# Kernel tuning notes

Measured on AMD Instinct MI355X. Metric: run time of the kernel, lower is better.

The kernel has to match this reference:

```python
import jax, jax.numpy as jnp
import numpy as np

NUM_HASHES = 4
EMBEDDING_DIM = 256
K = 512
B_TABLE = 256  # self.B


def setup_inputs() -> dict:
    key = jax.random.key(0)
    k1, k2, k3 = jax.random.split(key, 3)
    x = jax.random.randint(k1, (16, 4096, NUM_HASHES), 0, K, dtype=jnp.int64)
    # nn.Embedding(K*num_hashes + num_hashes, 1)
    weight_table = jax.random.normal(k2, (K * NUM_HASHES + NUM_HASHES, 1), dtype=jnp.float32)
    # nn.EmbeddingBag(B+1, embedding_dim)
    emb_table = jax.random.normal(k3, (B_TABLE + 1, EMBEDDING_DIM), dtype=jnp.float32)
    return {"x": x, "weight_table": weight_table, "emb_table": emb_table}


def reference(x, weight_table, emb_table):
    # x: [batch, seq, num_hashes] int in [0, K)
    num_hashes = x.shape[-1]
    indices = x // 2                                   # [b, s, h] in [0, 256]
    offsets = jnp.arange(num_hashes, dtype=x.dtype) * (K + 1)
    weight_idx = x + offsets                           # [b, s, h]
    w = weight_table[weight_idx, 0]                    # [b, s, h] per-sample weights
    e = emb_table[indices]                             # [b, s, h, d]
    # EmbeddingBag mode='sum' with per_sample_weights: weighted sum over hashes
    return jnp.einsum('bsh,bshd->bsd', w, e)
```

## Files before the change

kernel.cpp:

```cpp
#include <hip/hip_runtime.h>

#define NUM_HASHES 4
#define DIM 256

typedef float v4f __attribute__((ext_vector_type(4)));

__global__ __launch_bounds__(256) void HashEmbedding_44976897523736_kernel(
    const int* __restrict__ x,
    const float* __restrict__ wt,
    const float* __restrict__ emb,
    float* __restrict__ out,
    int num_pos, int num_waves)
{
    const int lane = threadIdx.x & 63;
    const int wave = __builtin_amdgcn_readfirstlane(
        blockIdx.x * (blockDim.x >> 6) + (threadIdx.x >> 6));

    #pragma unroll 2
    for (int p = wave; p < num_pos; p += num_waves) {
        const int4 xi = *reinterpret_cast<const int4*>(x + p * NUM_HASHES);
        const int i0 = __builtin_amdgcn_readfirstlane(xi.x);
        const int i1 = __builtin_amdgcn_readfirstlane(xi.y);
        const int i2 = __builtin_amdgcn_readfirstlane(xi.z);
        const int i3 = __builtin_amdgcn_readfirstlane(xi.w);

        const float w0 = wt[i0];
        const float w1 = wt[i1 + 513];
        const float w2 = wt[i2 + 1026];
        const float w3 = wt[i3 + 1539];

        const v4f e0 = reinterpret_cast<const v4f*>(emb + (i0 >> 1) * DIM)[lane];
        const v4f e1 = reinterpret_cast<const v4f*>(emb + (i1 >> 1) * DIM)[lane];
        const v4f e2 = reinterpret_cast<const v4f*>(emb + (i2 >> 1) * DIM)[lane];
        const v4f e3 = reinterpret_cast<const v4f*>(emb + (i3 >> 1) * DIM)[lane];

        v4f r = w0 * e0 + w1 * e1 + w2 * e2 + w3 * e3;

        __builtin_nontemporal_store(
            r, reinterpret_cast<v4f*>(out + (size_t)p * DIM) + lane);
    }
}

extern "C" void kernel_launch(void* const* d_in, const int* in_sizes, int n_in,
                              void* d_out, int out_size, void* d_ws, size_t ws_size,
                              hipStream_t stream) {
    const int*   x   = (const int*)d_in[0];
    const float* wt  = (const float*)d_in[1];
    const float* emb = (const float*)d_in[2];
    float*       out = (float*)d_out;

    const int num_pos = in_sizes[0] / NUM_HASHES;

    const int block = 256;
    int blocks = 2048;
    int num_waves = blocks * (block / 64);
    if (num_waves > num_pos) {
        blocks = (num_pos * 64 + block - 1) / block;
        if (blocks < 1) blocks = 1;
        num_waves = blocks * (block / 64);
    }

    HashEmbedding_44976897523736_kernel<<<blocks, block, 0, stream>>>(
        x, wt, emb, out, num_pos, num_waves);
}
```

Baseline: 85.18 us.

## Stage embedding table slices in LDS and split output columns across blocks

Each block loads a 64-column slice of the embedding table into shared memory and serves gathers from LDS, with blocks split across four column slices. This aims to replace global/L2 gather traffic with LDS reads. In exchange, index and weight loads are repeated per slice, stores narrow to scalar floats, and the large LDS footprint with 1024-thread blocks limits occupancy.

```diff
diff --git a/kernel.cpp b/kernel.cpp
--- a/kernel.cpp
+++ b/kernel.cpp
@@ -2,22 +2,39 @@
 
 #define NUM_HASHES 4
 #define DIM 256
+#define SLICE 64
+#define NSLICES (DIM / SLICE)
+#define LDS_ROWS 256
+#define BLOCK 1024
+#define WPB (BLOCK / 64)
 
-typedef float v4f __attribute__((ext_vector_type(4)));
-
-__global__ __launch_bounds__(256) void HashEmbedding_44976897523736_kernel(
+__global__ __launch_bounds__(BLOCK) void HashEmbedding_44976897523736_kernel(
     const int* __restrict__ x,
     const float* __restrict__ wt,
     const float* __restrict__ emb,
     float* __restrict__ out,
-    int num_pos, int num_waves)
+    int num_pos, int waves_per_slice)
 {
-    const int lane = threadIdx.x & 63;
-    const int wave = __builtin_amdgcn_readfirstlane(
-        blockIdx.x * (blockDim.x >> 6) + (threadIdx.x >> 6));
+    __shared__ float tbl[LDS_ROWS * SLICE];
 
-    #pragma unroll 2
-    for (int p = wave; p < num_pos; p += num_waves) {
+    const int tid   = threadIdx.x;
+    const int lane  = tid & 63;
+    const int slice = blockIdx.x & (NSLICES - 1);
+    const int chunk = blockIdx.x >> 2;
+
+    const float* esrc = emb + slice * SLICE;
+    #pragma unroll
+    for (int i = tid; i < LDS_ROWS * SLICE; i += BLOCK) {
+        const int r = i >> 6;
+        const int c = i & (SLICE - 1);
+        tbl[i] = esrc[r * DIM + c];
+    }
+    __syncthreads();
+
+    const int wave = __builtin_amdgcn_readfirstlane(chunk * WPB + (tid >> 6));
+
+    #pragma unroll 4
+    for (int p = wave; p < num_pos; p += waves_per_slice) {
         const int4 xi = *reinterpret_cast<const int4*>(x + p * NUM_HASHES);
         const int i0 = __builtin_amdgcn_readfirstlane(xi.x);
         const int i1 = __builtin_amdgcn_readfirstlane(xi.y);
@@ -29,15 +46,15 @@
         const float w2 = wt[i2 + 1026];
         const float w3 = wt[i3 + 1539];
 
-        const v4f e0 = reinterpret_cast<const v4f*>(emb + (i0 >> 1) * DIM)[lane];
-        const v4f e1 = reinterpret_cast<const v4f*>(emb + (i1 >> 1) * DIM)[lane];
-        const v4f e2 = reinterpret_cast<const v4f*>(emb + (i2 >> 1) * DIM)[lane];
-        const v4f e3 = reinterpret_cast<const v4f*>(emb + (i3 >> 1) * DIM)[lane];
+        const float e0 = tbl[(i0 >> 1) * SLICE + lane];
+        const float e1 = tbl[(i1 >> 1) * SLICE + lane];
+        const float e2 = tbl[(i2 >> 1) * SLICE + lane];
+        const float e3 = tbl[(i3 >> 1) * SLICE + lane];
 
-        v4f r = w0 * e0 + w1 * e1 + w2 * e2 + w3 * e3;
+        const float r = w0 * e0 + w1 * e1 + w2 * e2 + w3 * e3;
 
         __builtin_nontemporal_store(
-            r, reinterpret_cast<v4f*>(out + (size_t)p * DIM) + lane);
+            r, out + (size_t)p * DIM + slice * SLICE + lane);
     }
 }
 
@@ -51,15 +68,14 @@
 
     const int num_pos = in_sizes[0] / NUM_HASHES;
 
-    const int block = 256;
-    int blocks = 2048;
-    int num_waves = blocks * (block / 64);
-    if (num_waves > num_pos) {
-        blocks = (num_pos * 64 + block - 1) / block;
-        if (blocks < 1) blocks = 1;
-        num_waves = blocks * (block / 64);
+    int chunks = 128;
+    if (chunks * WPB > num_pos) {
+        chunks = (num_pos + WPB - 1) / WPB;
+        if (chunks < 1) chunks = 1;
     }
+    const int waves_per_slice = chunks * WPB;
+    const int blocks = chunks * NSLICES;
 
-    HashEmbedding_44976897523736_kernel<<<blocks, block, 0, stream>>>(
-        x, wt, emb, out, num_pos, num_waves);
+    HashEmbedding_44976897523736_kernel<<<blocks, BLOCK, 0, stream>>>(
+        x, wt, emb, out, num_pos, waves_per_slice);
 }
```

Result: slower. 99.74 us (+17.1%).

## Stage embedding table in LDS as fp16 and use 1024-thread blocks

Applied to the files above, without the earlier changes.

Each block converts the first 256 rows of the embedding table to fp16 and stores them in a 128 KB shared-memory array. The per-position gathers then read 8-byte fp16 vectors from LDS instead of 16-byte fp32 vectors from global memory/L2. The launch shape changes to 256 blocks of 1024 threads, which fits one block per CU. The cost is a per-block table preload of the full table from global memory, plus reduced embedding precision from the fp16 rounding.

```diff
diff --git a/kernel.cpp b/kernel.cpp
--- a/kernel.cpp
+++ b/kernel.cpp
@@ -2,19 +2,38 @@
 
 #define NUM_HASHES 4
 #define DIM 256
+#define ROWS 256
+#define BLOCK 1024
+#define WPB (BLOCK / 64)
 
-typedef float v4f __attribute__((ext_vector_type(4)));
+typedef float     v4f __attribute__((ext_vector_type(4)));
+typedef _Float16  h4  __attribute__((ext_vector_type(4)));
 
-__global__ __launch_bounds__(256) void HashEmbedding_44976897523736_kernel(
+__global__ __launch_bounds__(BLOCK) void HashEmbedding_44976897523736_kernel(
     const int* __restrict__ x,
     const float* __restrict__ wt,
     const float* __restrict__ emb,
     float* __restrict__ out,
     int num_pos, int num_waves)
 {
-    const int lane = threadIdx.x & 63;
+    __shared__ _Float16 tbl[ROWS * DIM];
+
+    const int tid  = threadIdx.x;
+    const int lane = tid & 63;
+
+    for (int i = tid; i < ROWS * DIM / 4; i += BLOCK) {
+        const v4f v = reinterpret_cast<const v4f*>(emb)[i];
+        h4 h;
+        h[0] = (_Float16)v[0];
+        h[1] = (_Float16)v[1];
+        h[2] = (_Float16)v[2];
+        h[3] = (_Float16)v[3];
+        reinterpret_cast<h4*>(tbl)[i] = h;
+    }
+    __syncthreads();
+
     const int wave = __builtin_amdgcn_readfirstlane(
-        blockIdx.x * (blockDim.x >> 6) + (threadIdx.x >> 6));
+        blockIdx.x * WPB + (tid >> 6));
 
     #pragma unroll 2
     for (int p = wave; p < num_pos; p += num_waves) {
@@ -29,12 +48,16 @@
         const float w2 = wt[i2 + 1026];
         const float w3 = wt[i3 + 1539];
 
-        const v4f e0 = reinterpret_cast<const v4f*>(emb + (i0 >> 1) * DIM)[lane];
-        const v4f e1 = reinterpret_cast<const v4f*>(emb + (i1 >> 1) * DIM)[lane];
-        const v4f e2 = reinterpret_cast<const v4f*>(emb + (i2 >> 1) * DIM)[lane];
-        const v4f e3 = reinterpret_cast<const v4f*>(emb + (i3 >> 1) * DIM)[lane];
+        const h4 e0 = reinterpret_cast<const h4*>(tbl)[((i0 >> 1) << 6) + lane];
+        const h4 e1 = reinterpret_cast<const h4*>(tbl)[((i1 >> 1) << 6) + lane];
+        const h4 e2 = reinterpret_cast<const h4*>(tbl)[((i2 >> 1) << 6) + lane];
+        const h4 e3 = reinterpret_cast<const h4*>(tbl)[((i3 >> 1) << 6) + lane];
 
-        v4f r = w0 * e0 + w1 * e1 + w2 * e2 + w3 * e3;
+        v4f r;
+        #pragma unroll
+        for (int j = 0; j < 4; ++j)
+            r[j] = w0 * (float)e0[j] + w1 * (float)e1[j]
+                 + w2 * (float)e2[j] + w3 * (float)e3[j];
 
         __builtin_nontemporal_store(
             r, reinterpret_cast<v4f*>(out + (size_t)p * DIM) + lane);
@@ -51,15 +74,14 @@
 
     const int num_pos = in_sizes[0] / NUM_HASHES;
 
-    const int block = 256;
-    int blocks = 2048;
-    int num_waves = blocks * (block / 64);
+    int blocks = 256;
+    int num_waves = blocks * WPB;
     if (num_waves > num_pos) {
-        blocks = (num_pos * 64 + block - 1) / block;
+        blocks = (num_pos + WPB - 1) / WPB;
         if (blocks < 1) blocks = 1;
-        num_waves = blocks * (block / 64);
+        num_waves = blocks * WPB;
     }
 
-    HashEmbedding_44976897523736_kernel<<<blocks, block, 0, stream>>>(
+    HashEmbedding_44976897523736_kernel<<<blocks, BLOCK, 0, stream>>>(
         x, wt, emb, out, num_pos, num_waves);
 }
```

Result: slower. 90.25 us (+6.0%).
